# Kernel optimization log

Hardware: AMD Instinct MI355X
Metric: run time of the kernel (lower is better)

The kernel has to match this reference:

```python
import jax, jax.numpy as jnp
import numpy as np

NP = 8           # Np: prediction horizon
NUM_LAYERS = 2
HIDDEN = 1024    # hidden_dim
FEAT = 128       # input_dim == output_dim == nFeatures (closed-loop feedback)
NSAMPLES = 96
BATCH = 128


def setup_inputs() -> dict:
    key = jax.random.key(0)
    ks = jax.random.split(key, 13)
    s = 1.0 / np.sqrt(HIDDEN)
    u = lambda k, shape: jax.random.uniform(k, shape, jnp.float32, -s, s)
    return {
        "inMusic": jax.random.normal(ks[0], (NSAMPLES, BATCH, FEAT), jnp.float32),
        "h0": 0.1 * jax.random.normal(ks[1], (NUM_LAYERS, BATCH, HIDDEN), jnp.float32),
        "c0": 0.1 * jax.random.normal(ks[2], (NUM_LAYERS, BATCH, HIDDEN), jnp.float32),
        "W_ih_l0": u(ks[3], (4 * HIDDEN, FEAT)),
        "W_hh_l0": u(ks[4], (4 * HIDDEN, HIDDEN)),
        "b_ih_l0": u(ks[5], (4 * HIDDEN,)),
        "b_hh_l0": u(ks[6], (4 * HIDDEN,)),
        "W_ih_l1": u(ks[7], (4 * HIDDEN, HIDDEN)),
        "W_hh_l1": u(ks[8], (4 * HIDDEN, HIDDEN)),
        "b_ih_l1": u(ks[9], (4 * HIDDEN,)),
        "b_hh_l1": u(ks[10], (4 * HIDDEN,)),
        "W_lin": u(ks[11], (FEAT, HIDDEN)),
        "b_lin": u(ks[12], (FEAT,)),
    }


def _cell(x, h, c, Wih, Whh, bih, bhh):
    # PyTorch LSTM cell, gate order i, f, g, o
    g = x @ Wih.T + bih + h @ Whh.T + bhh                 # [B, 4H]
    i, f, gg, o = jnp.split(g, 4, axis=-1)
    c2 = jax.nn.sigmoid(f) * c + jax.nn.sigmoid(i) * jnp.tanh(gg)
    h2 = jax.nn.sigmoid(o) * jnp.tanh(c2)
    return h2, c2


def _forward(inMusic, h0, c0, W_ih_l0, W_hh_l0, b_ih_l0, b_hh_l0,
             W_ih_l1, W_hh_l1, b_ih_l1, b_hh_l1, W_lin, b_lin):
    nS, B, F = inMusic.shape
    layers = ((W_ih_l0, W_hh_l0, b_ih_l0, b_hh_l0),
              (W_ih_l1, W_hh_l1, b_ih_l1, b_hh_l1))

    @jax.checkpoint
    def stack_step(x, h, c):
        hs, cs, inp = [], [], x
        for li, (Wih, Whh, bih, bhh) in enumerate(layers):
            h2, c2 = _cell(inp, h[li], c[li], Wih, Whh, bih, bhh)
            hs.append(h2); cs.append(c2); inp = h2
        return jnp.stack(hs), jnp.stack(cs), inp

    linear = lambda x: x @ W_lin.T + b_lin

    def outer(carry, xs):
        hF, cF = carry
        xk, k = xs
        # filtering step (inner n == 0); runs only when min(k, Np) >= 1, i.e. k >= 1
        h1, c1, top = stack_step(xk, hF, cF)
        upd = k >= 1
        hF2 = jnp.where(upd, h1, hF)
        cF2 = jnp.where(upd, c1, cF)
        pred0 = linear(top)

        # closed-loop prediction steps n = 1..Np-1 (each reads the previous
        # step's linear output, which is what outMusic[k+n,:,:,n-1] holds)
        def inner(pc, _):
            hp, cp, pred = pc
            h2, c2, t2 = stack_step(pred, hp, cp)
            p2 = linear(t2)
            return (h2, c2, p2), p2

        _, preds_rest = jax.lax.scan(inner, (h1, c1, pred0), None, length=NP - 1)
        preds_k = jnp.concatenate([pred0[None], preds_rest], axis=0)   # [Np, B, F]
        return (hF2, cF2), (preds_k, pred0)

    (hF, cF), (preds, pred0s) = jax.lax.scan(outer, (h0, c0), (inMusic, jnp.arange(nS)))

    # triangular init: outMusic[k, :, :, n] = inMusic[k] for k < Np, n >= k
    tri = jnp.arange(NP)[:, None] <= jnp.arange(NP)[None, :]           # [k, n]
    fill = jnp.where(tri[:, None, None, :], inMusic[:NP, :, :, None], 0.0)
    outMusic = jnp.zeros((nS, B, F, NP), inMusic.dtype).at[:NP].set(fill)

    # scatter: outMusic[k+n+1, :, :, n] = preds[k, n] iff n < min(k, Np) and k+n+1 < nS
    kk = jnp.arange(nS)[:, None]
    nn = jnp.arange(NP)[None, :]
    rows = kk + nn + 1
    valid = (nn < jnp.minimum(kk, NP)) & (rows < nS)
    rows = jnp.where(valid, rows, nS).reshape(-1)                      # OOB -> dropped
    cols = jnp.broadcast_to(nn, (nS, NP)).reshape(-1)
    outMusic = outMusic.at[rows, :, :, cols].set(preds.reshape(nS * NP, B, F), mode="drop")

    nextSampleEst = pred0s[-1][None]                                   # [1, B, F]
    return outMusic, hF, cF, nextSampleEst


def reference(inMusic, h0, c0, W_ih_l0, W_hh_l0, b_ih_l0, b_hh_l0,
              W_ih_l1, W_hh_l1, b_ih_l1, b_hh_l1, W_lin, b_lin):
    return _forward(inMusic, h0, c0, W_ih_l0, W_hh_l0, b_ih_l0, b_hh_l0,
                    W_ih_l1, W_hh_l1, b_ih_l1, b_hh_l1, W_lin, b_lin)
```

## Files before the change

kernel.cpp:

```cpp
#include <hip/hip_runtime.h>

#define HID 1024
#define FEAT 128
#define BAT 128
#define NSAMP 96
#define NPRED 8
#define GD 4096
#define SLOTE ((size_t)BAT * HID)
#define PREDT 16384
#define CHUNK 8192

typedef unsigned short u16;
typedef unsigned int u32;
typedef unsigned long long u64;
typedef short bf16x8 __attribute__((ext_vector_type(8)));
typedef float f32x4 __attribute__((ext_vector_type(4)));

__device__ inline u16 f2bf(float f) {
    unsigned u = __float_as_uint(f);
    u += 0x7FFFu + ((u >> 16) & 1u);
    return (u16)(u >> 16);
}
__device__ inline float bf2f(u16 h) { return __uint_as_float(((unsigned)h) << 16); }
__device__ inline float fsig(float x) { return 1.0f / (1.0f + __expf(-x)); }
__device__ inline float ftanh(float x) { return 1.0f - 2.0f / (__expf(2.0f * x) + 1.0f); }

__device__ inline size_t fmoff(int row, int kk) {
    return (size_t)(kk >> 6) * CHUNK + (size_t)(row >> 6) * 4096
         + (size_t)((row >> 4) & 3) * 1024 + (size_t)((kk >> 5) & 1) * 512
         + (size_t)((kk >> 3) & 3) * 128 + (size_t)(row & 15) * 8 + (kk & 7);
}

__device__ inline void gl2lds16(const u16* g, u16* l) {
    __builtin_amdgcn_global_load_lds(
        (const __attribute__((address_space(1))) u32*)g,
        (__attribute__((address_space(3))) u32*)l, 16, 0, 0);
}

__device__ inline void cstore8(u16* p, u64 v) {
    __hip_atomic_store((__attribute__((address_space(1))) u64*)p, v,
                       __ATOMIC_RELAXED, __HIP_MEMORY_SCOPE_AGENT);
}

__device__ inline u64 pack4bf(u16 a, u16 b, u16 c, u16 d) {
    return (u64)a | ((u64)b << 16) | ((u64)c << 32) | ((u64)d << 48);
}

#define FLAGN (2 * 97 * 32 * 32)
__device__ inline void waitset(const int* base) {
    const int tid = threadIdx.x;
    if (tid < 64) {
        long t = 0;
        for (;;) {
            int v = (tid < 32)
                ? __hip_atomic_load(base + tid * 32, __ATOMIC_RELAXED, __HIP_MEMORY_SCOPE_AGENT)
                : 1;
            if (__all(v != 0)) break;
            __builtin_amdgcn_s_sleep(2);
            if (++t > 3000000L) break;
        }
    }
    __builtin_amdgcn_fence(__ATOMIC_ACQUIRE, "workgroup");
    __syncthreads();
}

__device__ inline size_t pgoff(int q, int cp, int lane) {
    return (size_t)(q >> 1) * CHUNK
         + (size_t)(((cp >> 2) * 8) + ((cp & 3) * 2) + (q & 1)) * 512 + lane * 8;
}

union SMemA {
    u16 st[4][2][4096];
    float g[32][132];
};

__global__ __launch_bounds__(256, 1) void lstm_chain(
    const u16* __restrict__ inb,
    const u16* __restrict__ Wih0p, const u16* __restrict__ Whh0p,
    const u16* __restrict__ Wih1p, const u16* __restrict__ Whh1p,
    const float* __restrict__ bp0, const float* __restrict__ bp1,
    const float* __restrict__ c0,
    u16* __restrict__ chainH, u16* __restrict__ chainCb,
    float* __restrict__ h_std, float* __restrict__ c_std,
    int* __restrict__ flags)
{
    __shared__ SMemA sm;
    const int blk = blockIdx.x;
    const int l = blk >> 5, tn = blk & 31;
    const int tid = threadIdx.x;
    const int wave = tid >> 6, lane = tid & 63;
    const int wm = wave >> 1, wn = wave & 1;
    const int quad = lane >> 4, lc = lane & 15;
    const int rl = tid >> 3, ub = (tid & 7) * 4;

    const u16* BihS = (l ? Wih1p : Wih0p) + (size_t)tn * 128 * (l ? HID : FEAT);
    const u16* BhhS = (l ? Whh1p : Whh0p) + (size_t)tn * 128 * HID;
    const float* bias = l ? bp1 : bp0;
    auto fw = [&](int ll, int s) { return flags + ((size_t)(ll * 97 + s) * 32) * 32; };

    float creg[4][4];
#pragma unroll
    for (int i = 0; i < 4; ++i) {
        int lrow = (rl >> 4) * 64 + i * 16 + (rl & 15);
        float4 c4 = *(const float4*)(c0 + (size_t)l * SLOTE + (size_t)lrow * HID + tn * 32 + ub);
        creg[i][0] = c4.x; creg[i][1] = c4.y; creg[i][2] = c4.z; creg[i][3] = c4.w;
    }
    float bv[4];
#pragma unroll
    for (int j = 0; j < 4; ++j) bv[j] = bias[tn * 128 + wn * 64 + j * 16 + lc];

    const int frA = wm * 2048 + (quad * 16 + lc) * 8;
    const int frB = wn * 2048 + (quad * 16 + lc) * 8;

    for (int k = 0; k < NSAMP; ++k) {
        const int rk = (k <= 1) ? 0 : k;

        const u16 *A0, *B0, *A1s, *B1s; int KP0, NP;
        if (l == 0) {
            A0 = inb + (size_t)k * PREDT;              B0 = BihS; KP0 = 4;
            A1s = chainH + (size_t)rk * SLOTE;         B1s = BhhS; NP = 36;
        } else {
            A0 = chainH + (size_t)(k + 1) * SLOTE;     B0 = BihS; KP0 = 32;
            A1s = chainH + (size_t)(97 + rk) * SLOTE;  B1s = BhhS; NP = 64;
        }
        auto issue = [&](int q, int buf) {
            const u16 *Ab, *Bb; int qq;
            if (q < KP0) { Ab = A0;  Bb = B0;  qq = q; }
            else         { Ab = A1s; Bb = B1s; qq = q - KP0; }
#pragma unroll
            for (int c2 = 0; c2 < 2; ++c2) {
                int cp = wave * 2 + c2;
                size_t go = pgoff(qq, cp, lane);
                gl2lds16(Ab + go, &sm.st[buf][0][cp * 512]);
                gl2lds16(Bb + go, &sm.st[buf][1][cp * 512]);
            }
        };

        if (l == 0) {
            issue(0, 0); issue(1, 1); issue(2, 2);
            waitset(fw(0, rk));
        } else {
            waitset(fw(0, k + 1));
            issue(0, 0); issue(1, 1); issue(2, 2);
            waitset(fw(1, rk));
        }

        f32x4 acc[4][4];
#pragma unroll
        for (int j = 0; j < 4; ++j) {
            f32x4 bvv = {bv[j], bv[j], bv[j], bv[j]};
#pragma unroll
            for (int i = 0; i < 4; ++i) acc[i][j] = bvv;
        }

        for (int q = 0; q < NP; ++q) {
            if (q + 2 < NP)      asm volatile("s_waitcnt vmcnt(8)" ::: "memory");
            else if (q + 1 < NP) asm volatile("s_waitcnt vmcnt(4)" ::: "memory");
            else                 asm volatile("s_waitcnt vmcnt(0)" ::: "memory");
            __builtin_amdgcn_s_barrier();
            __builtin_amdgcn_sched_barrier(0);
            if (q + 3 < NP) issue(q + 3, (q + 3) & 3);
            const u16* la = sm.st[q & 3][0];
            const u16* lb = sm.st[q & 3][1];
            bf16x8 aF[4], bF[4];
#pragma unroll
            for (int i = 0; i < 4; ++i)
                aF[i] = *(const bf16x8*)&la[frA + i * 512];
#pragma unroll
            for (int j = 0; j < 4; ++j)
                bF[j] = *(const bf16x8*)&lb[frB + j * 512];
#pragma unroll
            for (int i = 0; i < 4; ++i)
#pragma unroll
                for (int j = 0; j < 4; ++j)
                    acc[i][j] = __builtin_amdgcn_mfma_f32_16x16x32_bf16(aF[i], bF[j], acc[i][j], 0, 0, 0);
        }

        __syncthreads();
        size_t slotBase = (size_t)(l * 97 + k + 1) * SLOTE;
#pragma unroll 1
        for (int i = 0; i < 4; ++i) {
#pragma unroll
            for (int j = 0; j < 4; ++j)
#pragma unroll
                for (int r = 0; r < 4; ++r)
                    sm.g[wm * 16 + quad * 4 + r][wn * 64 + j * 16 + lc] = acc[i][j][r];
            __syncthreads();
            int lrow = (rl >> 4) * 64 + i * 16 + (rl & 15);
            float c2v[4], h2v[4];
#pragma unroll
            for (int uu = 0; uu < 4; ++uu) {
                float4 gg = *(const float4*)&sm.g[rl][(ub + uu) * 4];
                float iv = fsig(gg.x), fv = fsig(gg.y), gv = ftanh(gg.z), ov = fsig(gg.w);
                float c2 = fv * creg[i][uu] + iv * gv;
                if (k != 0) creg[i][uu] = c2;
                c2v[uu] = c2;
                h2v[uu] = ov * ftanh(c2);
            }
            cstore8(chainH + slotBase + fmoff(lrow, tn * 32 + ub),
                    pack4bf(f2bf(h2v[0]), f2bf(h2v[1]), f2bf(h2v[2]), f2bf(h2v[3])));
            size_t pOff = slotBase + ((size_t)tn * 128 + lrow) * 32 + ub;
            *(ushort4*)(chainCb + pOff) =
                make_ushort4(f2bf(c2v[0]), f2bf(c2v[1]), f2bf(c2v[2]), f2bf(c2v[3]));
            if (k == 95) {
                size_t sOff = (size_t)l * SLOTE + (size_t)lrow * HID + tn * 32 + ub;
                *(float4*)(h_std + sOff) = make_float4(h2v[0], h2v[1], h2v[2], h2v[3]);
                *(float4*)(c_std + sOff) = make_float4(c2v[0], c2v[1], c2v[2], c2v[3]);
            }
            __syncthreads();
        }
        if (tid == 0)
            __hip_atomic_store((__attribute__((address_space(1))) int*)(fw(l, k + 1) + tn * 32),
                               1, __ATOMIC_RELAXED, __HIP_MEMORY_SCOPE_AGENT);
    }
}

struct GArgs {
    const u16* A1; const u16* A2;
    const u16 *B1, *B2;
    const float* bias;
    const u16* c_in; u16* cout_b;
    u16* h_out;
    u16* lin_out;
    int KP1, KP2;
    int as1, as2;
    int mode;
};

union SMemB {
    u16 st[3][2][4096];
    float g[32][132];
};

__global__ __launch_bounds__(256, 3) void gemm_lstm(GArgs g)
{
    __shared__ SMemB sm;
    const int tid = threadIdx.x;
    const int wave = tid >> 6, lane = tid & 63;
    const int wm = wave >> 1, wn = wave & 1;
    const int quad = lane >> 4, lc = lane & 15;
    const int tn = blockIdx.x & 31;
    const int tm0 = (blockIdx.x >> 5) * 4;
    const int frA = wm * 2048 + (quad * 16 + lc) * 8;
    const int frB = wn * 2048 + (quad * 16 + lc) * 8;

    const u16* B1p = g.B1 + (size_t)tn * g.KP1 * 4096;
    const u16* B2p = g.B2 + (size_t)tn * g.KP2 * 4096;
    const int NP = g.KP1 + g.KP2;

    for (int t = 0; t < 4; ++t) {
        const int tm = tm0 + t;
        const u16* A1t = g.A1 + (size_t)tm * g.as1;
        const u16* A2t = g.A2 + (size_t)tm * g.as2;

        auto issue = [&](int q, int buf) {
            const u16 *Ab, *Bb; int qq;
            if (q < g.KP1) { Ab = A1t; Bb = B1p; qq = q; }
            else           { Ab = A2t; Bb = B2p; qq = q - g.KP1; }
#pragma unroll
            for (int c2 = 0; c2 < 2; ++c2) {
                int cp = wave * 2 + c2;
                size_t go = pgoff(qq, cp, lane);
                gl2lds16(Ab + go, &sm.st[buf][0][cp * 512]);
                gl2lds16(Bb + go, &sm.st[buf][1][cp * 512]);
            }
        };

        f32x4 acc[4][4];
#pragma unroll
        for (int j = 0; j < 4; ++j) {
            float bvx = g.bias[tn * 128 + wn * 64 + j * 16 + lc];
            f32x4 bvv = {bvx, bvx, bvx, bvx};
#pragma unroll
            for (int i = 0; i < 4; ++i) acc[i][j] = bvv;
        }

        issue(0, 0);
        issue(1, 1);
        for (int q = 0; q < NP; ++q) {
            if (q + 1 < NP) asm volatile("s_waitcnt vmcnt(4)" ::: "memory");
            else            asm volatile("s_waitcnt vmcnt(0)" ::: "memory");
            __builtin_amdgcn_s_barrier();
            __builtin_amdgcn_sched_barrier(0);
            if (q + 2 < NP) issue(q + 2, (q + 2) % 3);
            const u16* la = sm.st[q % 3][0];
            const u16* lb = sm.st[q % 3][1];
            bf16x8 aF[4], bF[4];
#pragma unroll
            for (int i = 0; i < 4; ++i)
                aF[i] = *(const bf16x8*)&la[frA + i * 512];
#pragma unroll
            for (int j = 0; j < 4; ++j)
                bF[j] = *(const bf16x8*)&lb[frB + j * 512];
#pragma unroll
            for (int i = 0; i < 4; ++i)
#pragma unroll
                for (int j = 0; j < 4; ++j)
                    acc[i][j] = __builtin_amdgcn_mfma_f32_16x16x32_bf16(aF[i], bF[j], acc[i][j], 0, 0, 0);
        }
        __syncthreads();

        const int rl = tid >> 3, ub = (tid & 7) * 4;
#pragma unroll 1
        for (int i = 0; i < 4; ++i) {
#pragma unroll
            for (int j = 0; j < 4; ++j)
#pragma unroll
                for (int r = 0; r < 4; ++r)
                    sm.g[wm * 16 + quad * 4 + r][wn * 64 + j * 16 + lc] = acc[i][j][r];
            __syncthreads();
            int lrow = (rl >> 4) * 64 + i * 16 + (rl & 15);
            size_t pOff = (size_t)tm * SLOTE + ((size_t)tn * 128 + lrow) * 32 + ub;
            ushort4 co = *(const ushort4*)(g.c_in + pOff);
            float cold[4] = {bf2f(co.x), bf2f(co.y), bf2f(co.z), bf2f(co.w)};
            float c2v[4], h2v[4];
#pragma unroll
            for (int uu = 0; uu < 4; ++uu) {
                float4 gg = *(const float4*)&sm.g[rl][(ub + uu) * 4];
                float iv = fsig(gg.x), fv = fsig(gg.y), gv = ftanh(gg.z), ov = fsig(gg.w);
                float c2 = fv * cold[uu] + iv * gv;
                c2v[uu] = c2;
                h2v[uu] = ov * ftanh(c2);
            }
            *(ushort4*)(g.cout_b + pOff) =
                make_ushort4(f2bf(c2v[0]), f2bf(c2v[1]), f2bf(c2v[2]), f2bf(c2v[3]));
            *(ushort4*)(g.h_out + (size_t)tm * SLOTE + fmoff(lrow, tn * 32 + ub)) =
                make_ushort4(f2bf(h2v[0]), f2bf(h2v[1]), f2bf(h2v[2]), f2bf(h2v[3]));
            __syncthreads();
        }
    }
}

__global__ __launch_bounds__(256, 3) void gemm_lin(GArgs g)
{
    __shared__ u16 st[3][2][4096];
    const int tid = threadIdx.x;
    const int wave = tid >> 6, lane = tid & 63;
    const int wm = wave >> 1, wn = wave & 1;
    const int quad = lane >> 4, lc = lane & 15;
    const int tm = blockIdx.x;
    const int frA = wm * 2048 + (quad * 16 + lc) * 8;
    const int frB = wn * 2048 + (quad * 16 + lc) * 8;

    const u16* A1t = g.A1 + (size_t)tm * g.as1;
    const int NP = g.KP1;

    auto issue = [&](int q, int buf) {
#pragma unroll
        for (int c2 = 0; c2 < 2; ++c2) {
            int cp = wave * 2 + c2;
            size_t go = pgoff(q, cp, lane);
            gl2lds16(A1t + go, &st[buf][0][cp * 512]);
            gl2lds16(g.B1 + go, &st[buf][1][cp * 512]);
        }
    };

    f32x4 acc[4][4];
#pragma unroll
    for (int j = 0; j < 4; ++j) {
        float bvx = g.bias[wn * 64 + j * 16 + lc];
        f32x4 bvv = {bvx, bvx, bvx, bvx};
#pragma unroll
        for (int i = 0; i < 4; ++i) acc[i][j] = bvv;
    }

    issue(0, 0);
    issue(1, 1);
    for (int q = 0; q < NP; ++q) {
        if (q + 1 < NP) asm volatile("s_waitcnt vmcnt(4)" ::: "memory");
        else            asm volatile("s_waitcnt vmcnt(0)" ::: "memory");
        __builtin_amdgcn_s_barrier();
        __builtin_amdgcn_sched_barrier(0);
        if (q + 2 < NP) issue(q + 2, (q + 2) % 3);
        const u16* la = st[q % 3][0];
        const u16* lb = st[q % 3][1];
        bf16x8 aF[4], bF[4];
#pragma unroll
        for (int i = 0; i < 4; ++i)
            aF[i] = *(const bf16x8*)&la[frA + i * 512];
#pragma unroll
        for (int j = 0; j < 4; ++j)
            bF[j] = *(const bf16x8*)&lb[frB + j * 512];
#pragma unroll
        for (int i = 0; i < 4; ++i)
#pragma unroll
            for (int j = 0; j < 4; ++j)
                acc[i][j] = __builtin_amdgcn_mfma_f32_16x16x32_bf16(aF[i], bF[j], acc[i][j], 0, 0, 0);
    }

#pragma unroll
    for (int i = 0; i < 4; ++i)
#pragma unroll
        for (int j = 0; j < 4; ++j)
#pragma unroll
            for (int r = 0; r < 4; ++r) {
                int grow = wm * 64 + i * 16 + quad * 4 + r;
                int gcol = wn * 64 + j * 16 + lc;
                g.lin_out[(size_t)tm * PREDT + fmoff(grow, gcol)] = f2bf(acc[i][j][r]);
            }
}

__global__ void convert_weight(const float* __restrict__ src, u16* __restrict__ dst,
                               int kshift, int permute, int total) {
    int idx = blockIdx.x * 256 + threadIdx.x;
    if (idx >= total) return;
    const int K = 1 << kshift;
    int kk = idx & (K - 1);
    int rr = (idx >> kshift) & 127;
    int s = idx >> (kshift + 7);
    int jp = s * 128 + rr;
    int srow = permute ? ((jp & 3) * HID + (jp >> 2)) : jp;
    dst[((size_t)s << (kshift + 7)) + fmoff(rr, kk)] =
        f2bf(src[((size_t)srow << kshift) + kk]);
}

__global__ void conv_input(const float* __restrict__ in, u16* __restrict__ inb) {
    int idx = blockIdx.x * 256 + threadIdx.x;
    int f = idx & 127;
    int b = (idx >> 7) & 127;
    int k = idx >> 14;
    inb[(size_t)k * PREDT + fmoff(b, f)] = f2bf(in[idx]);
}

__global__ void combine_bias(const float* __restrict__ bi, const float* __restrict__ bh,
                             float* __restrict__ dst) {
    int j = blockIdx.x * 256 + threadIdx.x;
    int s = (j & 3) * HID + (j >> 2);
    dst[j] = bi[s] + bh[s];
}

__global__ void init_state(const float* __restrict__ h0, u16* __restrict__ chainH) {
    int idx = blockIdx.x * 256 + threadIdx.x;
    int l = idx >> 17;
    int r = idx & (int)(SLOTE - 1);
    int b = r >> 10, hh = r & 1023;
    chainH[(size_t)l * 97 * SLOTE + fmoff(b, hh)] = f2bf(h0[idx]);
}

__global__ void init_flags(int* __restrict__ f) {
    int gid = blockIdx.x * 256 + threadIdx.x;
    if (gid >= FLAGN) return;
    int step = (gid >> 10) % 97;
    f[gid] = ((gid & 31) == 0 && step == 0) ? 1 : 0;
}

__global__ void copy_next(const u16* __restrict__ predsb, float* __restrict__ out) {
    int idx = blockIdx.x * 256 + threadIdx.x;
    int b = idx >> 7, f = idx & 127;
    out[idx] = bf2f(predsb[(size_t)95 * PREDT + fmoff(b, f)]);
}

__global__ void gather_out(const float* __restrict__ inMusic, const u16* __restrict__ predsb,
                           float* __restrict__ outM) {
    int idx = blockIdx.x * 256 + threadIdx.x;
    int n = idx & 7;
    int f = (idx >> 3) & 127;
    int b = (idx >> 10) & 127;
    int r = idx >> 17;
    float v = 0.0f;
    if (r < NPRED && n >= r) {
        v = inMusic[((size_t)r * BAT + b) * FEAT + f];
    } else {
        int k = r - n - 1;
        if (n < k)
            v = bf2f(predsb[((size_t)n * NSAMP + k) * PREDT + fmoff(b, f)]);
    }
    outM[idx] = v;
}

__global__ void zero_out(float* __restrict__ o, int nmax) {
    int idx = blockIdx.x * 256 + threadIdx.x;
    if (idx < nmax) o[idx] = 0.0f;
}

extern "C" void kernel_launch(void* const* d_in, const int* in_sizes, int n_in,
                              void* d_out, int out_size, void* d_ws, size_t ws_size,
                              hipStream_t stream) {
    (void)in_sizes; (void)n_in;
    const float* inMusic = (const float*)d_in[0];
    const float* h0   = (const float*)d_in[1];
    const float* c0   = (const float*)d_in[2];
    const float* Wih0 = (const float*)d_in[3];
    const float* Whh0 = (const float*)d_in[4];
    const float* bih0 = (const float*)d_in[5];
    const float* bhh0 = (const float*)d_in[6];
    const float* Wih1 = (const float*)d_in[7];
    const float* Whh1 = (const float*)d_in[8];
    const float* bih1 = (const float*)d_in[9];
    const float* bhh1 = (const float*)d_in[10];
    const float* Wlin = (const float*)d_in[11];
    const float* blin = (const float*)d_in[12];
    float* out = (float*)d_out;

    const size_t OUT_H = (size_t)NSAMP * BAT * FEAT * NPRED;
    const size_t OUT_C = OUT_H + 2 * SLOTE;
    const size_t OUT_NEXT = OUT_C + 2 * SLOTE;

    char* ws = (char*)d_ws;
    size_t off = 0;
    auto alloc = [&](size_t bytes) {
        void* p = ws + off;
        off = (off + bytes + 255) & ~(size_t)255;
        return p;
    };
    u16* Wih0p = (u16*)alloc((size_t)GD * FEAT * 2);
    u16* Whh0p = (u16*)alloc((size_t)GD * HID * 2);
    u16* Wih1p = (u16*)alloc((size_t)GD * HID * 2);
    u16* Whh1p = (u16*)alloc((size_t)GD * HID * 2);
    u16* Wlinb = (u16*)alloc((size_t)FEAT * HID * 2);
    float* bp0 = (float*)alloc(GD * 4);
    float* bp1 = (float*)alloc(GD * 4);
    u16* chainH  = (u16*)alloc((size_t)2 * 97 * SLOTE * 2);
    u16* chainCb = (u16*)alloc((size_t)2 * 97 * SLOTE * 2);
    u16* hp2 = (u16*)alloc((size_t)2 * (size_t)NSAMP * SLOTE * 2);
    u16* predsb = (u16*)alloc((size_t)NPRED * NSAMP * PREDT * 2);
    u16* inb = (u16*)alloc((size_t)NSAMP * PREDT * 2);
    int* flags = (int*)alloc((size_t)FLAGN * 4);

    if (off > ws_size) {
        zero_out<<<(out_size + 255) / 256, 256, 0, stream>>>(out, out_size);
        return;
    }

    convert_weight<<<(GD * FEAT + 255) / 256, 256, 0, stream>>>(Wih0, Wih0p, 7, 1, GD * FEAT);
    convert_weight<<<(GD * HID + 255) / 256, 256, 0, stream>>>(Whh0, Whh0p, 10, 1, GD * HID);
    convert_weight<<<(GD * HID + 255) / 256, 256, 0, stream>>>(Wih1, Wih1p, 10, 1, GD * HID);
    convert_weight<<<(GD * HID + 255) / 256, 256, 0, stream>>>(Whh1, Whh1p, 10, 1, GD * HID);
    convert_weight<<<(FEAT * HID + 255) / 256, 256, 0, stream>>>(Wlin, Wlinb, 10, 0, FEAT * HID);
    conv_input<<<(NSAMP * BAT * FEAT) / 256, 256, 0, stream>>>(inMusic, inb);
    combine_bias<<<GD / 256, 256, 0, stream>>>(bih0, bhh0, bp0);
    combine_bias<<<GD / 256, 256, 0, stream>>>(bih1, bhh1, bp1);
    init_state<<<(int)(2 * SLOTE) / 256, 256, 0, stream>>>(h0, chainH);
    init_flags<<<(FLAGN + 255) / 256, 256, 0, stream>>>(flags);

    lstm_chain<<<64, 256, 0, stream>>>(
        inb, Wih0p, Whh0p, Wih1p, Whh1p, bp0, bp1, c0,
        chainH, chainCb, out + OUT_H, out + OUT_C, flags);

    auto Hs = [&](int l, int s) { return chainH + ((size_t)l * 97 + s) * SLOTE; };
    auto Cs = [&](int l, int s) { return chainCb + ((size_t)l * 97 + s) * SLOTE; };

    u16* hbuf0[2] = {Hs(0, 1), Hs(1, 1)};
    u16* hbuf1[2] = {hp2, hp2 + (size_t)NSAMP * SLOTE};
    u16* cB[2] = {Cs(0, 1), Cs(1, 1)};

    auto mkLin = [&](const u16* src, u16* dst) {
        GArgs a = {};
        a.A1 = src; a.KP1 = 32; a.as1 = (int)SLOTE; a.KP2 = 0;
        a.B1 = Wlinb; a.bias = blin;
        a.lin_out = dst; a.mode = 1;
        return a;
    };
    auto mkB = [&](int l, const u16* A1, int kp1, int as1, const u16* A2, u16* nxt) {
        GArgs a = {};
        a.A1 = A1; a.KP1 = kp1; a.as1 = as1;
        a.A2 = A2; a.KP2 = 32; a.as2 = (int)SLOTE;
        a.B1 = (l == 0) ? Wih0p : Wih1p; a.B2 = (l == 0) ? Whh0p : Whh1p;
        a.bias = (l == 0) ? bp0 : bp1;
        a.c_in = cB[l]; a.cout_b = cB[l];
        a.h_out = nxt; a.mode = 0;
        return a;
    };

    gemm_lin<<<96, 256, 0, stream>>>(mkLin(hbuf0[1], predsb));
    copy_next<<<(BAT * FEAT) / 256, 256, 0, stream>>>(predsb, out + OUT_NEXT);

    for (int n = 1; n < NPRED; ++n) {
        u16* cur0 = (n & 1) ? hbuf0[0] : hbuf1[0];
        u16* cur1 = (n & 1) ? hbuf0[1] : hbuf1[1];
        u16* nxt0 = (n & 1) ? hbuf1[0] : hbuf0[0];
        u16* nxt1 = (n & 1) ? hbuf1[1] : hbuf0[1];
        const u16* pin = predsb + (size_t)(n - 1) * NSAMP * PREDT;
        u16* pout = predsb + (size_t)n * NSAMP * PREDT;
        gemm_lstm<<<768, 256, 0, stream>>>(mkB(0, pin, 4, PREDT, cur0, nxt0));
        gemm_lstm<<<768, 256, 0, stream>>>(mkB(1, nxt0, 32, (int)SLOTE, cur1, nxt1));
        gemm_lin<<<96, 256, 0, stream>>>(mkLin(nxt1, pout));
    }

    gather_out<<<(NSAMP * BAT * FEAT * NPRED) / 256, 256, 0, stream>>>(inMusic, predsb, out);
}
```

Before: 7.839 ms.

## Defer inter-layer flag wait into the K loop and reorder layer-1 operands

Measured after the change: 7.708 ms. Within noise of the previous version (-1.7%).

```diff
diff --git a/kernel.cpp b/kernel.cpp
--- a/kernel.cpp
+++ b/kernel.cpp
@@ -47,7 +47,7 @@
 }
 
 #define FLAGN (2 * 97 * 32 * 32)
-__device__ inline void waitset(const int* base) {
+__device__ inline void pollflag(const int* base) {
     const int tid = threadIdx.x;
     if (tid < 64) {
         long t = 0;
@@ -56,12 +56,12 @@
                 ? __hip_atomic_load(base + tid * 32, __ATOMIC_RELAXED, __HIP_MEMORY_SCOPE_AGENT)
                 : 1;
             if (__all(v != 0)) break;
-            __builtin_amdgcn_s_sleep(2);
+            __builtin_amdgcn_s_sleep(1);
             if (++t > 3000000L) break;
         }
     }
-    __builtin_amdgcn_fence(__ATOMIC_ACQUIRE, "workgroup");
-    __syncthreads();
+    __builtin_amdgcn_s_barrier();
+    __builtin_amdgcn_sched_barrier(0);
 }
 
 __device__ inline size_t pgoff(int q, int cp, int lane) {
@@ -115,14 +115,19 @@
     for (int k = 0; k < NSAMP; ++k) {
         const int rk = (k <= 1) ? 0 : k;
 
-        const u16 *A0, *B0, *A1s, *B1s; int KP0, NP;
+        const u16 *A0, *B0, *A1s, *B1s; int KP0, NP; const int* gate;
         if (l == 0) {
             A0 = inb + (size_t)k * PREDT;              B0 = BihS; KP0 = 4;
             A1s = chainH + (size_t)rk * SLOTE;         B1s = BhhS; NP = 36;
+            gate = fw(0, rk);
         } else {
-            A0 = chainH + (size_t)(k + 1) * SLOTE;     B0 = BihS; KP0 = 32;
-            A1s = chainH + (size_t)(97 + rk) * SLOTE;  B1s = BhhS; NP = 64;
-        }
+            pollflag(fw(1, rk));
+            A0 = chainH + (size_t)(97 + rk) * SLOTE;   B0 = BhhS; KP0 = 32;
+            A1s = chainH + (size_t)(k + 1) * SLOTE;    B1s = BihS; NP = 64;
+            gate = fw(0, k + 1);
+        }
+        const int qgate = KP0 - 3;
+
         auto issue = [&](int q, int buf) {
             const u16 *Ab, *Bb; int qq;
             if (q < KP0) { Ab = A0;  Bb = B0;  qq = q; }
@@ -136,14 +141,7 @@
             }
         };
 
-        if (l == 0) {
-            issue(0, 0); issue(1, 1); issue(2, 2);
-            waitset(fw(0, rk));
-        } else {
-            waitset(fw(0, k + 1));
-            issue(0, 0); issue(1, 1); issue(2, 2);
-            waitset(fw(1, rk));
-        }
+        issue(0, 0); issue(1, 1); issue(2, 2);
 
         f32x4 acc[4][4];
 #pragma unroll
@@ -159,6 +157,7 @@
             else                 asm volatile("s_waitcnt vmcnt(0)" ::: "memory");
             __builtin_amdgcn_s_barrier();
             __builtin_amdgcn_sched_barrier(0);
+            if (q == qgate) pollflag(gate);
             if (q + 3 < NP) issue(q + 3, (q + 3) & 3);
             const u16* la = sm.st[q & 3][0];
             const u16* lb = sm.st[q & 3][1];
@@ -185,7 +184,9 @@
 #pragma unroll
                 for (int r = 0; r < 4; ++r)
                     sm.g[wm * 16 + quad * 4 + r][wn * 64 + j * 16 + lc] = acc[i][j][r];
-            __syncthreads();
+            asm volatile("s_waitcnt lgkmcnt(0)" ::: "memory");
+            __builtin_amdgcn_s_barrier();
+            __builtin_amdgcn_sched_barrier(0);
             int lrow = (rl >> 4) * 64 + i * 16 + (rl & 15);
             float c2v[4], h2v[4];
 #pragma unroll
@@ -207,8 +208,11 @@
                 *(float4*)(h_std + sOff) = make_float4(h2v[0], h2v[1], h2v[2], h2v[3]);
                 *(float4*)(c_std + sOff) = make_float4(c2v[0], c2v[1], c2v[2], c2v[3]);
             }
-            __syncthreads();
-        }
+            __builtin_amdgcn_s_barrier();
+            __builtin_amdgcn_sched_barrier(0);
+        }
+        asm volatile("s_waitcnt vmcnt(0)" ::: "memory");
+        __builtin_amdgcn_s_barrier();
         if (tid == 0)
             __hip_atomic_store((__attribute__((address_space(1))) int*)(fw(l, k + 1) + tn * 32),
                                1, __ATOMIC_RELAXED, __HIP_MEMORY_SCOPE_AGENT);
@@ -303,6 +307,11 @@
         const int rl = tid >> 3, ub = (tid & 7) * 4;
 #pragma unroll 1
         for (int i = 0; i < 4; ++i) {
+#pragma unroll
+            for (int j = 0; j < 4; ++j)
+#pragma unroll
+                for (int r = 0; r < 4; ++r)
+                    sG_alias: ;
 #pragma unroll
             for (int j = 0; j < 4; ++j)
 #pragma unroll
```
